# Performance work log

Measured on AMD Instinct MI355X. Metric: run time of the kernel, lower is better.

## Reference

```python
import jax, jax.numpy as jnp
import numpy as np

BS, HW, HIDDEN, TOK, NTOK = 32, 1024, 256, 768, 2048


def setup_inputs() -> dict:
    key = jax.random.key(0)
    ks = jax.random.split(key, 6)
    s = 0.02  # init scale for weights
    return {
        "src": jax.random.normal(ks[0], (HW, BS, HIDDEN), jnp.float32),
        "codebook": jax.random.normal(ks[1], (NTOK, TOK), jnp.float32),
        "w_head": jax.random.normal(ks[2], (TOK, HIDDEN), jnp.float32) * s,
        "w_tail": jax.random.normal(ks[3], (HIDDEN, TOK), jnp.float32) * s,
        "w_pos": jax.random.normal(ks[4], (TOK, TOK), jnp.float32) * s,
        "b_pos": jnp.zeros((TOK,), jnp.float32),
        "w_gate": jax.random.normal(ks[5], (2, 2 * TOK), jnp.float32) * s,
        "h": 32,
        "w": 32,
    }


def reference(src, codebook, w_head, w_tail, w_pos, b_pos, w_gate, h, w):
    N, bs, hidden = src.shape  # [num_visu_token, bs, hidden_dim]
    tok = codebook.shape[1]
    # permute(1,2,0).view(bs,-1,h,w)
    x = jnp.transpose(src, (1, 2, 0)).reshape(bs, hidden, h, w)
    # conv_head: 1x1 conv, no bias
    xq = jnp.einsum("bchw,oc->bohw", x, w_head)  # [bs, tok, h, w]
    # raw-memory reshape, matches torch .view(-1, token_dim)
    flat = xq.reshape(-1, tok)  # [bs*h*w, tok]
    d = (
        jnp.sum(flat * flat, axis=1, keepdims=True)
        - 2.0 * flat @ codebook.T
        + jnp.sum(codebook * codebook, axis=1)[None, :]
    )
    indices = jnp.argmin(d, axis=1)  # [bs*h*w]
    quantized = codebook[indices]  # gather
    # straight-through estimator
    quantized = flat + jax.lax.stop_gradient(quantized - flat)
    # pos_align linear
    quantized = quantized @ w_pos.T + b_pos
    # view(bs, N, tok).permute(0,2,1).view(bs,-1,h,w)
    emb = jnp.transpose(quantized.reshape(bs, N, tok), (0, 2, 1)).reshape(bs, tok, h, w)
    # gated fusion
    gate_in = jnp.concatenate([emb, xq], axis=1)  # [bs, 2*tok, h, w]
    scores = jax.nn.softmax(jnp.einsum("bchw,oc->bohw", gate_in, w_gate), axis=1)
    fused = emb * scores[:, 0:1] + xq * scores[:, 1:2]
    # conv_tail 1x1, then flatten(2).permute(2,0,1)
    out = jnp.einsum("bchw,oc->bohw", fused, w_tail)  # [bs, hidden, h, w]
    out = jnp.transpose(out.reshape(bs, hidden, -1), (2, 0, 1))  # [h*w, bs, hidden]
    return out, indices
```

## Files before the change

kernel.cpp:

```cpp
#include <hip/hip_runtime.h>
#include <cstdint>

#define BSZ 32
#define NVIS 1024
#define HID 256
#define TOKD 768
#define NCODE 2048
#define NPIX 32768

typedef unsigned short u16;
typedef _Float16 half8 __attribute__((ext_vector_type(8)));
typedef unsigned short ushort8 __attribute__((ext_vector_type(8)));
using f32x4 = __attribute__((ext_vector_type(4))) float;

#define AS1 __attribute__((address_space(1)))
#define AS3 __attribute__((address_space(3)))

__device__ __forceinline__ f32x4 mfmaF16(half8 a, half8 b, f32x4 c) {
  return __builtin_amdgcn_mfma_f32_16x16x32_f16(a, b, c, 0, 0, 0);
}

__device__ __forceinline__ unsigned long long pack_key(float d, int idx) {
  unsigned int b = __float_as_uint(d);
  b = (b & 0x80000000u) ? ~b : (b | 0x80000000u);
  return ((unsigned long long)b << 32) | (unsigned int)idx;
}

__device__ __forceinline__ void split16(float v, u16& h, u16& l) {
  union { _Float16 f; u16 u; } a, b;
  a.f = (_Float16)v;
  float hf = (float)a.f;
  b.f = (_Float16)(v - hf);
  h = a.u; l = b.u;
}

__global__ __launch_bounds__(256)
void prep1(const float* __restrict__ cb, const float* __restrict__ wh,
           const float* __restrict__ wt, const float* __restrict__ wp,
           const float* __restrict__ wg, const float* __restrict__ bp,
           u16* __restrict__ cbh, u16* __restrict__ cbl,
           u16* __restrict__ whh, u16* __restrict__ whl,
           float* __restrict__ cbn, float* __restrict__ Mm, float* __restrict__ uv,
           float* __restrict__ Gt, float* __restrict__ g2,
           float* __restrict__ ct0, float* __restrict__ cg) {
  const int bid = blockIdx.x, tid = threadIdx.x;
  if (bid < 6144) {
    int i = bid*256 + tid;
    u16 h, l; split16(cb[i], h, l);
    cbh[i] = h; cbl[i] = l;
  } else if (bid < 6912) {
    int i = (bid - 6144)*256 + tid;
    u16 h, l; split16(wh[i], h, l);
    whh[i] = h; whl[i] = l;
  } else if (bid < 7424) {
    int n = (bid - 6912)*4 + (tid >> 6);
    int lane = tid & 63;
    float a = 0.f;
#pragma unroll
    for (int i = 0; i < 12; ++i) { float v = cb[(long)n*TOKD + lane + 64*i]; a += v*v; }
#pragma unroll
    for (int off = 32; off; off >>= 1) a += __shfl_down(a, off);
    if (lane == 0) cbn[n] = a;
  } else if (bid < 7680) {
    int c2 = bid - 7424, c1 = tid;
    float acc = 0.f;
    for (int t = 0; t < TOKD; ++t) acc += wh[t*HID + c1] * wt[(long)c2*TOKD + t];
    Mm[c1*HID + c2] = acc;
  } else if (bid < 7682) {
    int o = bid - 7680, c1 = tid;
    float acc = 0.f;
    for (int t = 0; t < TOKD; ++t) acc += wh[t*HID + c1] * wg[o*(2*TOKD) + TOKD + t];
    uv[o*HID + c1] = acc;
  } else if (bid < 8450) {
    int rbid = bid - 7682;
    int c = rbid & 255, part = rbid >> 8;
    int tp = part*256 + tid;
    float acc = 0.f;
    for (int t = 0; t < TOKD; ++t) acc += wt[(long)c*TOKD + t] * wp[(long)t*TOKD + tp];
    Gt[(long)tp*HID + c] = acc;
  } else if (bid < 8453) {
    int tp = (bid - 8450)*256 + tid;
    float a0 = 0.f, a1 = 0.f;
    for (int t = 0; t < TOKD; ++t) {
      float wv = wp[(long)t*TOKD + tp];
      a0 += wv * wg[t];
      a1 += wv * wg[2*TOKD + t];
    }
    g2[tp] = a0; g2[TOKD + tp] = a1;
  } else if (bid < 8454) {
    int c = tid;
    float a = 0.f;
    for (int t = 0; t < TOKD; ++t) a += bp[t] * wt[(long)c*TOKD + t];
    ct0[c] = a;
  } else {
    int o = tid >> 6, lane = tid & 63;
    if (o < 2) {
      float a = 0.f;
      for (int t = lane; t < TOKD; t += 64) a += bp[t] * wg[o*(2*TOKD) + t];
#pragma unroll
      for (int off = 32; off; off >>= 1) a += __shfl_down(a, off);
      if (lane == 0) cg[o] = a;
    }
  }
}

__global__ __launch_bounds__(256)
void prep2(const float* __restrict__ cb, const float* __restrict__ Gt,
           const float* __restrict__ ct0, const float* __restrict__ g2,
           const float* __restrict__ cg, float* __restrict__ tc,
           float* __restrict__ gA) {
  __shared__ float cbs[8][TOKD];
  const int n0 = blockIdx.x * 8, tid = threadIdx.x;
  for (int i = tid; i < 8*TOKD; i += 256) cbs[i / TOKD][i % TOKD] = cb[(long)n0*TOKD + i];
  __syncthreads();
  float acc[8] = {};
  for (int t = 0; t < TOKD; ++t) {
    float gv = Gt[(long)t*HID + tid];
#pragma unroll
    for (int i = 0; i < 8; ++i) acc[i] += cbs[i][t] * gv;
  }
  float c0v = ct0[tid];
#pragma unroll
  for (int i = 0; i < 8; ++i) tc[(long)(n0+i)*HID + tid] = acc[i] + c0v;
  {
    int i = tid >> 5, l32 = tid & 31;
    float a0 = 0.f, a1 = 0.f;
    for (int t = l32; t < TOKD; t += 32) {
      float cv = cbs[i][t];
      a0 += cv * g2[t];
      a1 += cv * g2[TOKD + t];
    }
#pragma unroll
    for (int off = 16; off; off >>= 1) { a0 += __shfl_down(a0, off); a1 += __shfl_down(a1, off); }
    if (l32 == 0) { gA[n0+i] = a0 + cg[0]; gA[NCODE + n0+i] = a1 + cg[1]; }
  }
}

__global__ __launch_bounds__(256)
void head_mfma(const u16* __restrict__ whh, const u16* __restrict__ whl,
               const float* __restrict__ src,
               u16* __restrict__ xqh, u16* __restrict__ xql) {
  __shared__ u16 SM[32768] __attribute__((aligned(16)));
  u16* Ah = SM;
  u16* Al = SM + 8192;
  u16* Bh = SM + 16384;
  u16* Bl = SM + 24576;
  const int tid = threadIdx.x, lane = tid & 63, w = tid >> 6;
  const int n = lane & 15, q = lane >> 4;
  const int rh = w & 1, ch = w >> 1;
  const int obase = blockIdx.x * 128, pbase = blockIdx.y * 128, b = blockIdx.z;

  auto stageA = [&](int kc, int buf) {
#pragma unroll
    for (int is = 0; is < 2; ++is) {
      int c = is*256 + tid;
      int t = c >> 6, qq = (c >> 4) & 3, nn = c & 15;
      long off = (long)(obase + t*16 + nn)*HID + kc*32 + qq*8;
      __builtin_amdgcn_global_load_lds((AS1 void*)(whh + off),
          (AS3 void*)&Ah[buf*4096 + c*8], 16, 0, 0);
      __builtin_amdgcn_global_load_lds((AS1 void*)(whl + off),
          (AS3 void*)&Al[buf*4096 + c*8], 16, 0, 0);
    }
  };
  auto stageB = [&](int kc, int buf) {
#pragma unroll
    for (int is = 0; is < 2; ++is) {
      int c = is*256 + tid;
      int t = c >> 6, qq = (c >> 4) & 3, nn = c & 15;
      const float* gp = src + ((long)(pbase + t*16 + nn)*BSZ + b)*HID + kc*32 + qq*8;
      float4 v0 = *(const float4*)gp;
      float4 v1 = *(const float4*)(gp + 4);
      float vv[8] = {v0.x, v0.y, v0.z, v0.w, v1.x, v1.y, v1.z, v1.w};
      ushort8 hv, lv;
#pragma unroll
      for (int j = 0; j < 8; ++j) { u16 hs, ls; split16(vv[j], hs, ls); hv[j] = hs; lv[j] = ls; }
      *(ushort8*)&Bh[buf*4096 + c*8] = hv;
      *(ushort8*)&Bl[buf*4096 + c*8] = lv;
    }
  };

  f32x4 acc[4][4];
#pragma unroll
  for (int i = 0; i < 4; ++i)
#pragma unroll
    for (int j = 0; j < 4; ++j) acc[i][j] = (f32x4){0.f, 0.f, 0.f, 0.f};

  stageA(0, 0); stageB(0, 0);
  __syncthreads();

  for (int kt = 0; kt < HID/32; ++kt) {
    const int buf = kt & 1;
    if (kt + 1 < HID/32) { stageA(kt + 1, buf ^ 1); stageB(kt + 1, buf ^ 1); }
    half8 af[4][2], bf[4][2];
#pragma unroll
    for (int rt = 0; rt < 4; ++rt) {
      int idx = buf*4096 + ((rh*4 + rt)*64 + q*16 + n)*8;
      af[rt][0] = *(const half8*)&Ah[idx];
      af[rt][1] = *(const half8*)&Al[idx];
    }
#pragma unroll
    for (int ct = 0; ct < 4; ++ct) {
      int idx = buf*4096 + ((ch*4 + ct)*64 + q*16 + n)*8;
      bf[ct][0] = *(const half8*)&Bh[idx];
      bf[ct][1] = *(const half8*)&Bl[idx];
    }
#pragma unroll
    for (int rt = 0; rt < 4; ++rt)
#pragma unroll
      for (int ct = 0; ct < 4; ++ct) {
        acc[rt][ct] = mfmaF16(af[rt][0], bf[ct][0], acc[rt][ct]);
        acc[rt][ct] = mfmaF16(af[rt][0], bf[ct][1], acc[rt][ct]);
        acc[rt][ct] = mfmaF16(af[rt][1], bf[ct][0], acc[rt][ct]);
      }
    __syncthreads();
  }

#pragma unroll
  for (int pass = 0; pass < 2; ++pass) {
    u16* dst = pass ? xql : xqh;
#pragma unroll
    for (int rt = 0; rt < 4; ++rt)
#pragma unroll
      for (int ct = 0; ct < 4; ++ct)
#pragma unroll
        for (int reg = 0; reg < 4; ++reg) {
          u16 hs, ls; split16(acc[rt][ct][reg], hs, ls);
          int ol = rh*64 + rt*16 + q*4 + reg;
          int pl = ch*64 + ct*16 + n;
          SM[ol*136 + pl] = pass ? ls : hs;
        }
    __syncthreads();
#pragma unroll
    for (int s = 0; s < 8; ++s) {
      int cc = tid*8 + s;
      int o = cc >> 4, p8 = cc & 15;
      ushort8 v = *(const ushort8*)&SM[o*136 + p8*8];
      *(ushort8*)(dst + ((long)b*TOKD + obase + o)*NVIS + pbase + p8*8) = v;
    }
    __syncthreads();
  }
}

__global__ __launch_bounds__(256)
void retile(u16* __restrict__ bufH, u16* __restrict__ bufL) {
  __shared__ u16 T[96*136] __attribute__((aligned(16)));
  const long tile = blockIdx.x;
  const int tid = threadIdx.x;
#pragma unroll
  for (int pass = 0; pass < 2; ++pass) {
    u16* buf = pass ? bufL : bufH;
    if (pass) __syncthreads();
#pragma unroll
    for (int i = 0; i < 6; ++i) {
      int g = i*256 + tid;
      int row = g / 96, c16 = g % 96;
      ushort8 v = *(const ushort8*)(buf + tile*12288 + row*768 + c16*8);
      *(ushort8*)&T[c16*136 + row*8] = v;
    }
    __syncthreads();
#pragma unroll
    for (int i = 0; i < 6; ++i) {
      int g = i*256 + tid;
      int kc = g >> 6, lp = g & 63;
      int q = lp >> 4, n = lp & 15;
      ushort8 v = *(const ushort8*)&T[(kc*4 + q)*136 + n*8];
      *(ushort8*)(buf + tile*12288 + (long)kc*512 + lp*8) = v;
    }
  }
}

__global__ __launch_bounds__(256, 2)
void vq_mfma(const u16* __restrict__ xqh, const u16* __restrict__ xql,
             const u16* __restrict__ cbh, const u16* __restrict__ cbl,
             const float* __restrict__ cbn, unsigned long long* __restrict__ keys) {
  __shared__ u16 SM[24576] __attribute__((aligned(16)));
  const int bid = blockIdx.x;
  const int xcd = bid & 7, slot = bid >> 3;
  const int rowBlk = xcd * 16 + (slot >> 4);
  const int codeBlk = slot & 15;
  const int rowTile0 = rowBlk * 16;
  const int codeTile0 = codeBlk * 8;
  const int tid = threadIdx.x, lane = tid & 63, w = tid >> 6;
  const int n = lane & 15, q = lane >> 4;
  const int wr = w >> 1, wc = w & 1;

  const size_t aOff = (size_t)(rowTile0 + 4*w) * 12288 + lane*8;
  const size_t bOff = (size_t)(codeTile0 + 2*w) * 12288 + lane*8;
  const int aChunk = (4*w)*512 + lane*8;
  const int bChunk = (2*w)*512 + lane*8;

  auto STAGE = [&](int ht, int buf) {
    const int seg = (ht >= 48) ? 2 : ((ht >= 24) ? 1 : 0);
    const int kk = ht - seg * 24;
    const u16* pa = ((seg == 1) ? xql : xqh) + aOff + kk*512;
    const u16* pb = ((seg == 2) ? cbl : cbh) + bOff + kk*512;
    u16* la = &SM[buf*8192 + aChunk];
    u16* lb = &SM[16384 + buf*4096 + bChunk];
    __builtin_amdgcn_global_load_lds((AS1 void*)pa,             (AS3 void*)la,          16, 0, 0);
    __builtin_amdgcn_global_load_lds((AS1 void*)(pa + 12288),   (AS3 void*)(la + 512),  16, 0, 0);
    __builtin_amdgcn_global_load_lds((AS1 void*)(pa + 2*12288), (AS3 void*)(la + 1024), 16, 0, 0);
    __builtin_amdgcn_global_load_lds((AS1 void*)(pa + 3*12288), (AS3 void*)(la + 1536), 16, 0, 0);
    __builtin_amdgcn_global_load_lds((AS1 void*)pb,             (AS3 void*)lb,          16, 0, 0);
    __builtin_amdgcn_global_load_lds((AS1 void*)(pb + 12288),   (AS3 void*)(lb + 512),  16, 0, 0);
  };

  f32x4 acc[8][4];
#pragma unroll
  for (int a = 0; a < 8; ++a)
#pragma unroll
    for (int b2 = 0; b2 < 4; ++b2) acc[a][b2] = (f32x4){0.f, 0.f, 0.f, 0.f};

  STAGE(0, 0);
  __syncthreads();

#pragma unroll 1
  for (int ht = 0; ht < 72; ++ht) {
    const int buf = ht & 1;
    if (ht < 71) STAGE(ht + 1, buf ^ 1);
    half8 Af[8], Bf[4];
    const int ab = buf*8192 + (wr*8)*512 + lane*8;
    const int bb = 16384 + buf*4096 + (wc*4)*512 + lane*8;
#pragma unroll
    for (int rt = 0; rt < 8; ++rt) Af[rt] = *(const half8*)&SM[ab + rt*512];
#pragma unroll
    for (int ct = 0; ct < 4; ++ct) Bf[ct] = *(const half8*)&SM[bb + ct*512];
    __builtin_amdgcn_s_setprio(1);
#pragma unroll
    for (int rt = 0; rt < 8; ++rt)
#pragma unroll
      for (int ct = 0; ct < 4; ++ct)
        acc[rt][ct] = mfmaF16(Af[rt], Bf[ct], acc[rt][ct]);
    __builtin_amdgcn_s_setprio(0);
    __syncthreads();
  }

  float cbv[4];
#pragma unroll
  for (int ct = 0; ct < 4; ++ct) cbv[ct] = cbn[(codeTile0 + wc*4 + ct)*16 + n];
#pragma unroll
  for (int rt = 0; rt < 8; ++rt) {
#pragma unroll
    for (int reg = 0; reg < 4; ++reg) {
      float bd = 3.4e38f; int bi = 0;
#pragma unroll
      for (int ct = 0; ct < 4; ++ct) {
        float d = cbv[ct] - 2.0f * acc[rt][ct][reg];
        int code = (codeTile0 + wc*4 + ct)*16 + n;
        if (d < bd) { bd = d; bi = code; }
      }
      unsigned long long k = pack_key(bd, bi);
      unsigned long long v;
      v = __shfl_xor(k, 1); k = (v < k) ? v : k;
      v = __shfl_xor(k, 2); k = (v < k) ? v : k;
      v = __shfl_xor(k, 4); k = (v < k) ? v : k;
      v = __shfl_xor(k, 8); k = (v < k) ? v : k;
      if (n == 0) {
        int row = (rowTile0 + wr*8 + rt)*16 + q*4 + reg;
        atomicMin(&keys[row], k);
      }
    }
  }
}

__global__ __launch_bounds__(256)
void fuse_out(const float* __restrict__ src, const unsigned long long* __restrict__ keys,
              const float* __restrict__ gA, const float* __restrict__ uvec,
              const float* __restrict__ Mm, const float* __restrict__ tailcode,
              float* __restrict__ out, float* __restrict__ outIdx) {
  __shared__ float ss[32][257];
  __shared__ float s0s[32];
  __shared__ int ids[32];
  const int tid = threadIdx.x;
  const int rb = blockIdx.x * 32;
  const int b = rb >> 10;
  const int p0 = rb & 1023;
#pragma unroll
  for (int qq = 0; qq < 32; ++qq)
    ss[qq][tid] = src[(long)(p0 + qq) * (BSZ*HID) + b*HID + tid];
  if (tid < 32) {
    unsigned long long u = keys[rb + tid];
    int id = (int)(unsigned int)(u & 0xFFFFFFFFull);
    ids[tid] = id;
    outIdx[rb + tid] = (float)id;
  }
  __syncthreads();
  {
    const int wv = tid >> 6, lane = tid & 63;
    for (int qq = 0; qq < 8; ++qq) {
      int qp = wv*8 + qq;
      float a0 = 0.f, a1 = 0.f;
#pragma unroll
      for (int i = 0; i < 4; ++i) {
        float v = ss[qp][lane + 64*i];
        a0 += v * uvec[lane + 64*i];
        a1 += v * uvec[HID + lane + 64*i];
      }
#pragma unroll
      for (int off = 32; off; off >>= 1) { a0 += __shfl_down(a0, off); a1 += __shfl_down(a1, off); }
      if (lane == 0) {
        int id = ids[qp];
        float l0 = gA[id] + a0;
        float l1 = gA[NCODE + id] + a1;
        s0s[qp] = 1.0f / (1.0f + expf(l1 - l0));
      }
    }
  }
  __syncthreads();
  const int qg = tid >> 5, cg = tid & 31;
  const int q0 = qg * 4, c0 = cg * 8;
  float acc[4][8] = {};
  for (int cp = 0; cp < HID; ++cp) {
    float4 m0 = *(const float4*)(Mm + cp*HID + c0);
    float4 m1 = *(const float4*)(Mm + cp*HID + c0 + 4);
    float mm[8] = {m0.x,m0.y,m0.z,m0.w,m1.x,m1.y,m1.z,m1.w};
#pragma unroll
    for (int i = 0; i < 4; ++i) {
      float sv = ss[q0+i][cp];
#pragma unroll
      for (int j = 0; j < 8; ++j) acc[i][j] += sv * mm[j];
    }
  }
#pragma unroll
  for (int i = 0; i < 4; ++i) {
    int qp = q0 + i;
    int id = ids[qp];
    float s0 = s0s[qp], s1 = 1.0f - s0;
    const float* tc = tailcode + (long)id*HID + c0;
    float* op = out + (long)(p0+qp)*(BSZ*HID) + b*HID + c0;
    float4 o0, o1;
    o0.x = s0*tc[0] + s1*acc[i][0]; o0.y = s0*tc[1] + s1*acc[i][1];
    o0.z = s0*tc[2] + s1*acc[i][2]; o0.w = s0*tc[3] + s1*acc[i][3];
    o1.x = s0*tc[4] + s1*acc[i][4]; o1.y = s0*tc[5] + s1*acc[i][5];
    o1.z = s0*tc[6] + s1*acc[i][6]; o1.w = s0*tc[7] + s1*acc[i][7];
    *(float4*)(op) = o0; *(float4*)(op+4) = o1;
  }
}

extern "C" void kernel_launch(void* const* d_in, const int* in_sizes, int n_in,
                              void* d_out, int out_size, void* d_ws, size_t ws_size,
                              hipStream_t stream) {
  const float* src    = (const float*)d_in[0];
  const float* cb     = (const float*)d_in[1];
  const float* w_head = (const float*)d_in[2];
  const float* w_tail = (const float*)d_in[3];
  const float* w_pos  = (const float*)d_in[4];
  const float* b_pos  = (const float*)d_in[5];
  const float* w_gate = (const float*)d_in[6];
  float* out = (float*)d_out;

  char* wsp = (char*)d_ws;
  size_t off = 0;
  auto alloc = [&](size_t bytes) {
    off = (off + 255) & ~(size_t)255;
    void* p = wsp + off; off += bytes; return p;
  };
  u16* xqh = (u16*)alloc((size_t)BSZ*TOKD*NVIS*2);
  u16* xql = (u16*)alloc((size_t)BSZ*TOKD*NVIS*2);
  u16* cbh = (u16*)alloc((size_t)NCODE*TOKD*2);
  u16* cbl = (u16*)alloc((size_t)NCODE*TOKD*2);
  u16* whh = (u16*)alloc((size_t)TOKD*HID*2);
  u16* whl = (u16*)alloc((size_t)TOKD*HID*2);
  float* cbn      = (float*)alloc((size_t)NCODE*4);
  float* Gt       = (float*)alloc((size_t)TOKD*HID*4);
  float* g2       = (float*)alloc((size_t)2*TOKD*4);
  float* ct0      = (float*)alloc((size_t)HID*4);
  float* cg       = (float*)alloc((size_t)2*4);
  float* tailcode = (float*)alloc((size_t)NCODE*HID*4);
  float* gA       = (float*)alloc((size_t)2*NCODE*4);
  float* Mm       = (float*)alloc((size_t)HID*HID*4);
  float* uvec     = (float*)alloc((size_t)2*HID*4);
  unsigned long long* keys = (unsigned long long*)alloc((size_t)NPIX*8);
  (void)ws_size; (void)in_sizes; (void)n_in; (void)out_size;

  prep1<<<8455, 256, 0, stream>>>(cb, w_head, w_tail, w_pos, w_gate, b_pos,
                                  cbh, cbl, whh, whl, cbn, Mm, uvec, Gt, g2, ct0, cg);
  retile<<<NCODE/16, 256, 0, stream>>>(cbh, cbl);
  prep2<<<NCODE/8, 256, 0, stream>>>(cb, Gt, ct0, g2, cg, tailcode, gA);

  head_mfma<<<dim3(TOKD/128, NVIS/128, BSZ), 256, 0, stream>>>(whh, whl, src, xqh, xql);
  retile<<<NPIX/16, 256, 0, stream>>>(xqh, xql);

  hipMemsetAsync(keys, 0xFF, (size_t)NPIX*8, stream);
  vq_mfma<<<2048, 256, 0, stream>>>(xqh, xql, cbh, cbl, cbn, keys);

  fuse_out<<<NPIX/32, 256, 0, stream>>>(src, keys, gA, uvec, Mm, tailcode,
                                        out, out + (size_t)NVIS*BSZ*HID);
}
```

Baseline: 707.3 us.

## Load A fragments directly to registers and deepen codebook LDS pipeline

The VQ distance kernel now has each wave load its own 4 row-tiles of A straight from global memory into registers, and no longer stages them through LDS. Each wave now covers all 8 code tiles instead of a 2x2 wave split. Only the codebook B tiles go through LDS, now in a 4-deep ring with a prefetch distance of 2. Waits use explicit vmcnt so loads overlap the MFMAs. This removes LDS traffic and capacity for A and shrinks shared memory, which may raise occupancy. The cost is more register pressure, and A must now be read without reuse across waves.

New measurement: 657.4 us. 1.08x faster.

```diff
diff --git a/kernel.cpp b/kernel.cpp
--- a/kernel.cpp
+++ b/kernel.cpp
@@ -273,7 +273,7 @@
 void vq_mfma(const u16* __restrict__ xqh, const u16* __restrict__ xql,
              const u16* __restrict__ cbh, const u16* __restrict__ cbl,
              const float* __restrict__ cbn, unsigned long long* __restrict__ keys) {
-  __shared__ u16 SM[24576] __attribute__((aligned(16)));
+  __shared__ u16 SM[16384] __attribute__((aligned(16)));
   const int bid = blockIdx.x;
   const int xcd = bid & 7, slot = bid >> 3;
   const int rowBlk = xcd * 16 + (slot >> 4);
@@ -282,70 +282,81 @@
   const int codeTile0 = codeBlk * 8;
   const int tid = threadIdx.x, lane = tid & 63, w = tid >> 6;
   const int n = lane & 15, q = lane >> 4;
-  const int wr = w >> 1, wc = w & 1;
-
-  const size_t aOff = (size_t)(rowTile0 + 4*w) * 12288 + lane*8;
+
+  const u16* paH = xqh + (size_t)(rowTile0 + 4*w) * 12288 + lane*8;
+  const u16* paL = xql + (size_t)(rowTile0 + 4*w) * 12288 + lane*8;
   const size_t bOff = (size_t)(codeTile0 + 2*w) * 12288 + lane*8;
-  const int aChunk = (4*w)*512 + lane*8;
   const int bChunk = (2*w)*512 + lane*8;
 
-  auto STAGE = [&](int ht, int buf) {
-    const int seg = (ht >= 48) ? 2 : ((ht >= 24) ? 1 : 0);
-    const int kk = ht - seg * 24;
-    const u16* pa = ((seg == 1) ? xql : xqh) + aOff + kk*512;
-    const u16* pb = ((seg == 2) ? cbl : cbh) + bOff + kk*512;
-    u16* la = &SM[buf*8192 + aChunk];
-    u16* lb = &SM[16384 + buf*4096 + bChunk];
-    __builtin_amdgcn_global_load_lds((AS1 void*)pa,             (AS3 void*)la,          16, 0, 0);
-    __builtin_amdgcn_global_load_lds((AS1 void*)(pa + 12288),   (AS3 void*)(la + 512),  16, 0, 0);
-    __builtin_amdgcn_global_load_lds((AS1 void*)(pa + 2*12288), (AS3 void*)(la + 1024), 16, 0, 0);
-    __builtin_amdgcn_global_load_lds((AS1 void*)(pa + 3*12288), (AS3 void*)(la + 1536), 16, 0, 0);
-    __builtin_amdgcn_global_load_lds((AS1 void*)pb,             (AS3 void*)lb,          16, 0, 0);
-    __builtin_amdgcn_global_load_lds((AS1 void*)(pb + 12288),   (AS3 void*)(lb + 512),  16, 0, 0);
+  auto STAGE_B = [&](int ht, int buf) {
+    const int kk = ht - ((ht >= 48) ? 48 : ((ht >= 24) ? 24 : 0));
+    const u16* pb = ((ht >= 48) ? cbl : cbh) + bOff + kk*512;
+    u16* lb = &SM[buf*4096 + bChunk];
+    __builtin_amdgcn_global_load_lds((AS1 void*)pb,           (AS3 void*)lb,         16, 0, 0);
+    __builtin_amdgcn_global_load_lds((AS1 void*)(pb + 12288), (AS3 void*)(lb + 512), 16, 0, 0);
   };
 
-  f32x4 acc[8][4];
-#pragma unroll
-  for (int a = 0; a < 8; ++a)
-#pragma unroll
-    for (int b2 = 0; b2 < 4; ++b2) acc[a][b2] = (f32x4){0.f, 0.f, 0.f, 0.f};
-
-  STAGE(0, 0);
-  __syncthreads();
+  auto LOAD_A = [&](int ht, half8 (&R)[4]) {
+    const int sA = (ht >= 24 && ht < 48);
+    const int kA = ht - ((ht >= 48) ? 48 : (sA ? 24 : 0));
+    const u16* pa_ = (sA ? paL : paH) + kA*512;
+#pragma unroll
+    for (int i = 0; i < 4; ++i) R[i] = *(const half8*)(pa_ + (size_t)i*12288);
+  };
+
+  f32x4 acc[4][8];
+#pragma unroll
+  for (int a = 0; a < 4; ++a)
+#pragma unroll
+    for (int b2 = 0; b2 < 8; ++b2) acc[a][b2] = (f32x4){0.f, 0.f, 0.f, 0.f};
+
+  half8 Aa[4], Ab[4];
+
+  LOAD_A(0, Aa); STAGE_B(0, 0);
+  LOAD_A(1, Ab); STAGE_B(1, 1);
+  asm volatile("s_waitcnt vmcnt(0)" ::: "memory");
+  asm volatile("s_barrier" ::: "memory");
+
+#define VQ_ITER(HT, CUR)                                                     \
+  {                                                                          \
+    const int ht_ = (HT);                                                    \
+    const int pf_ = (ht_ + 2 > 71) ? 71 : ht_ + 2;                           \
+    STAGE_B(pf_, (ht_ + 2) & 3);                                             \
+    half8 Bf[8];                                                             \
+    const int bb = (ht_ & 3)*4096 + lane*8;                                  \
+    _Pragma("unroll")                                                        \
+    for (int ct = 0; ct < 8; ++ct) Bf[ct] = *(const half8*)&SM[bb + ct*512]; \
+    __builtin_amdgcn_s_setprio(1);                                           \
+    _Pragma("unroll")                                                        \
+    for (int rt = 0; rt < 4; ++rt)                                           \
+      _Pragma("unroll")                                                      \
+      for (int ct = 0; ct < 8; ++ct)                                         \
+        acc[rt][ct] = mfmaF16(CUR[rt], Bf[ct], acc[rt][ct]);                 \
+    __builtin_amdgcn_s_setprio(0);                                           \
+    LOAD_A(pf_, CUR);                  \
+    asm volatile("s_waitcnt vmcnt(6)" ::: "memory");    \
+    asm volatile("s_barrier" ::: "memory");             \
+  }
 
 #pragma unroll 1
-  for (int ht = 0; ht < 72; ++ht) {
-    const int buf = ht & 1;
-    if (ht < 71) STAGE(ht + 1, buf ^ 1);
-    half8 Af[8], Bf[4];
-    const int ab = buf*8192 + (wr*8)*512 + lane*8;
-    const int bb = 16384 + buf*4096 + (wc*4)*512 + lane*8;
-#pragma unroll
-    for (int rt = 0; rt < 8; ++rt) Af[rt] = *(const half8*)&SM[ab + rt*512];
-#pragma unroll
-    for (int ct = 0; ct < 4; ++ct) Bf[ct] = *(const half8*)&SM[bb + ct*512];
-    __builtin_amdgcn_s_setprio(1);
-#pragma unroll
-    for (int rt = 0; rt < 8; ++rt)
-#pragma unroll
-      for (int ct = 0; ct < 4; ++ct)
-        acc[rt][ct] = mfmaF16(Af[rt], Bf[ct], acc[rt][ct]);
-    __builtin_amdgcn_s_setprio(0);
-    __syncthreads();
-  }
-
-  float cbv[4];
-#pragma unroll
-  for (int ct = 0; ct < 4; ++ct) cbv[ct] = cbn[(codeTile0 + wc*4 + ct)*16 + n];
-#pragma unroll
-  for (int rt = 0; rt < 8; ++rt) {
+  for (int h2 = 0; h2 < 36; ++h2) {
+    VQ_ITER(2*h2,     Aa);
+    VQ_ITER(2*h2 + 1, Ab);
+  }
+#undef VQ_ITER
+
+  float cbv[8];
+#pragma unroll
+  for (int ct = 0; ct < 8; ++ct) cbv[ct] = cbn[(codeTile0 + ct)*16 + n];
+#pragma unroll
+  for (int rt = 0; rt < 4; ++rt) {
 #pragma unroll
     for (int reg = 0; reg < 4; ++reg) {
       float bd = 3.4e38f; int bi = 0;
 #pragma unroll
-      for (int ct = 0; ct < 4; ++ct) {
+      for (int ct = 0; ct < 8; ++ct) {
         float d = cbv[ct] - 2.0f * acc[rt][ct][reg];
-        int code = (codeTile0 + wc*4 + ct)*16 + n;
+        int code = (codeTile0 + ct)*16 + n;
         if (d < bd) { bd = d; bi = code; }
       }
       unsigned long long k = pack_key(bd, bi);
@@ -355,7 +366,7 @@
       v = __shfl_xor(k, 4); k = (v < k) ? v : k;
       v = __shfl_xor(k, 8); k = (v < k) ? v : k;
       if (n == 0) {
-        int row = (rowTile0 + wr*8 + rt)*16 + q*4 + reg;
+        int row = (rowTile0 + 4*w + rt)*16 + q*4 + reg;
         atomicMin(&keys[row], k);
       }
     }
```
